# Kernel tuning notes

Hardware: AMD Instinct MI355X
Metric: run time of the kernel (lower is better)

Reference implementation:

```python
import jax, jax.numpy as jnp
import numpy as np

N = 100000
IN_CH, HID_CH, OUT_CH = 128, 128, 64
E = 1600000


def gcn_layer(x, W, b, src, dst, num_nodes):
    """PyG GCNConv: add self-loops, symmetric deg^-1/2 normalization,
    x' = D^-1/2 (A+I) D^-1/2 (x W) + b."""
    # degrees including self-loops (deg = 1 + in-degree with unit edge weights)
    ones = jnp.ones(dst.shape[0], dtype=x.dtype)
    deg = jnp.ones(num_nodes, dtype=x.dtype).at[dst].add(ones)
    dinv = jax.lax.rsqrt(deg)
    h = x @ W  # [N, out_dim] -- transform before propagate (PyG order)
    # neighbor messages
    norm = dinv[src] * dinv[dst]                      # [E]
    msg = h[src] * norm[:, None]                      # [E, out_dim] (traffic-bound)
    agg = jax.ops.segment_sum(msg, dst, num_segments=num_nodes)
    # self-loop contribution: norm_ii = dinv[i]^2
    agg = agg + h * (dinv * dinv)[:, None]
    return agg + b


def setup_inputs() -> dict:
    key = jax.random.key(0)
    ks = jax.random.split(key, 7)
    x = jax.random.normal(ks[0], (N, IN_CH), dtype=jnp.float32)
    edge_index = jax.random.randint(ks[1], (2, E), 0, N, dtype=jnp.int64)
    # Glorot-style init like PyG GCNConv
    W1 = jax.random.normal(ks[2], (IN_CH, HID_CH), dtype=jnp.float32) * (1.0 / np.sqrt(IN_CH))
    b1 = jnp.zeros((HID_CH,), dtype=jnp.float32)
    W2 = jax.random.normal(ks[3], (HID_CH, OUT_CH), dtype=jnp.float32) * (1.0 / np.sqrt(HID_CH))
    b2 = jnp.zeros((OUT_CH,), dtype=jnp.float32)
    return {"x": x, "edge_index": edge_index, "W1": W1, "b1": b1, "W2": W2, "b2": b2}


def reference(x, edge_index, W1, b1, W2, b2):
    src, dst = edge_index[0], edge_index[1]
    h = gcn_layer(x, W1, b1, src, dst, N)
    h = jax.nn.relu(h)  # dropout is identity in eval mode
    out = gcn_layer(h, W2, b2, src, dst, N)
    return out
```

## Files before the change

kernel.cpp:

```cpp
#include <hip/hip_runtime.h>
#include <hip/hip_fp16.h>

#define NNODES 100000
#define NEDGES 1600000
#define IN_C   128
#define HID_C  128
#define OUT_C  64

#define XCD_COUNT   8
#define XCD_NODES   ((NNODES + XCD_COUNT - 1) / XCD_COUNT)
#define FILL_CHUNKS 256
#define EDGES_PER_CHUNK ((NEDGES + FILL_CHUNKS - 1) / FILL_CHUNKS)

#define CAP     64
#define OVF_MAX 4096

typedef __attribute__((ext_vector_type(8))) _Float16 half8;
typedef __attribute__((ext_vector_type(4))) _Float16 half4;
typedef __attribute__((ext_vector_type(4))) float floatx4;

__device__ __forceinline__ long long load_idx(const void* p, long long i, int is64) {
  return is64 ? ((const long long*)p)[i] : (long long)((const int*)p)[i];
}

__global__ void detect_idx_kernel(const void* eidx, int* flag) {
  const unsigned* w = (const unsigned*)eidx;
  int lane = threadIdx.x & 63;
  unsigned v = w[2 * lane + 1];
  unsigned long long bad = __ballot(v != 0u);
  if (lane == 0) *flag = (bad == 0ull) ? 1 : 0;
}


__global__ void zero_cnt_kernel(int* cnt, int* ovf_cnt) {
  int i = blockIdx.x * 256 + threadIdx.x;
  if (i < NNODES) cnt[i] = 0;
  if (i == 0) *ovf_cnt = 0;
}

__global__ void compress_kernel(const void* eidx, const int* __restrict__ flag,
                                int* __restrict__ src32, int* __restrict__ dst32) {
  int e = blockIdx.x * 256 + threadIdx.x;
  if (e < NEDGES) {
    int is64 = *flag;
    src32[e] = (int)load_idx(eidx, e, is64);
    dst32[e] = (int)load_idx(eidx, (long long)NEDGES + e, is64);
  }
}

__global__ __launch_bounds__(256) void fill_fused_kernel(const int* __restrict__ src32,
                                                         const int* __restrict__ dst32,
                                                         int* __restrict__ cnt,
                                                         int* __restrict__ pad_csr,
                                                         int* __restrict__ ovf_cnt,
                                                         int2* __restrict__ ovf) {
  const int xcd = blockIdx.x & (XCD_COUNT - 1);
  const int chunk = blockIdx.x >> 3;
  const int lo = xcd * XCD_NODES;
  const int e_beg = chunk * EDGES_PER_CHUNK;
  const int e_end = min(e_beg + EDGES_PER_CHUNK, NEDGES);
  for (int e = e_beg + threadIdx.x; e < e_end; e += 256) {
    int d = __builtin_nontemporal_load(&dst32[e]);
    if ((unsigned)(d - lo) < (unsigned)XCD_NODES) {
      int s = __builtin_nontemporal_load(&src32[e]);
      int k = atomicAdd(&cnt[d], 1);
      if (k < CAP) {
        pad_csr[d * CAP + k] = s;
      } else {
        int p = atomicAdd(ovf_cnt, 1);
        if (p < OVF_MAX) ovf[p] = make_int2(s, d);
      }
    }
  }
}

__global__ void rsqrt_deg_kernel(const int* __restrict__ cnt, float* __restrict__ dinv) {
  int i = blockIdx.x * 256 + threadIdx.x;
  if (i < NNODES) dinv[i] = rsqrtf((float)(cnt[i] + 1));
}

struct F8 {
  float x0, x1, x2, x3, x4, x5, x6, x7;
};

__device__ __forceinline__ void add_h8(F8& a, const __half* p) {
  int4 r = *(const int4*)p;
  const __half2* h = (const __half2*)&r;
  float2 f0 = __half22float2(h[0]);
  float2 f1 = __half22float2(h[1]);
  float2 f2 = __half22float2(h[2]);
  float2 f3 = __half22float2(h[3]);
  a.x0 += f0.x; a.x1 += f0.y; a.x2 += f1.x; a.x3 += f1.y;
  a.x4 += f2.x; a.x5 += f2.y; a.x6 += f3.x; a.x7 += f3.y;
}

template <int C, bool RELU, bool OUT16>
__global__ __launch_bounds__(256) void gather_kernel(const int* __restrict__ cnt,
                                                     const int* __restrict__ pad_csr,
                                                     const float* __restrict__ dinv,
                                                     const __half* __restrict__ Hs,
                                                     const float* __restrict__ bias,
                                                     const int* __restrict__ ovf_cnt,
                                                     const int2* __restrict__ ovf,
                                                     void* __restrict__ OutPtr) {
  constexpr int TPN = C / 8;
  int gid = blockIdx.x * 256 + threadIdx.x;
  int i = gid / TPN;
  int c8 = (gid % TPN) * 8;
  if (i >= NNODES) return;

  const float di = dinv[i];
  const int deg = cnt[i];
  const int beg = i * CAP;
  const int end = beg + min(deg, CAP);
  const int* __restrict__ lst = pad_csr;

  F8 a0 = {}, a1 = {}, a2 = {}, a3 = {};
  add_h8(a0, &Hs[(size_t)i * C + c8]);

  int j = beg;
  for (; j + 8 <= end; j += 8) {
    int s0 = lst[j + 0], s1 = lst[j + 1], s2 = lst[j + 2], s3 = lst[j + 3];
    int s4 = lst[j + 4], s5 = lst[j + 5], s6 = lst[j + 6], s7 = lst[j + 7];
    add_h8(a0, &Hs[(size_t)s0 * C + c8]);
    add_h8(a1, &Hs[(size_t)s1 * C + c8]);
    add_h8(a2, &Hs[(size_t)s2 * C + c8]);
    add_h8(a3, &Hs[(size_t)s3 * C + c8]);
    add_h8(a0, &Hs[(size_t)s4 * C + c8]);
    add_h8(a1, &Hs[(size_t)s5 * C + c8]);
    add_h8(a2, &Hs[(size_t)s6 * C + c8]);
    add_h8(a3, &Hs[(size_t)s7 * C + c8]);
  }
  for (; j + 2 <= end; j += 2) {
    int s0 = lst[j + 0], s1 = lst[j + 1];
    add_h8(a0, &Hs[(size_t)s0 * C + c8]);
    add_h8(a1, &Hs[(size_t)s1 * C + c8]);
  }
  if (j < end) {
    add_h8(a0, &Hs[(size_t)lst[j] * C + c8]);
  }

  if (deg > CAP) {
    int n = min(*ovf_cnt, OVF_MAX);
    for (int t = 0; t < n; ++t) {
      int2 p = ovf[t];
      if (p.y == i) add_h8(a0, &Hs[(size_t)p.x * C + c8]);
    }
  }

  float s0 = a0.x0 + a1.x0 + a2.x0 + a3.x0;
  float s1 = a0.x1 + a1.x1 + a2.x1 + a3.x1;
  float s2 = a0.x2 + a1.x2 + a2.x2 + a3.x2;
  float s3 = a0.x3 + a1.x3 + a2.x3 + a3.x3;
  float s4 = a0.x4 + a1.x4 + a2.x4 + a3.x4;
  float s5 = a0.x5 + a1.x5 + a2.x5 + a3.x5;
  float s6 = a0.x6 + a1.x6 + a2.x6 + a3.x6;
  float s7 = a0.x7 + a1.x7 + a2.x7 + a3.x7;

  float4 b0 = *(const float4*)&bias[c8];
  float4 b1 = *(const float4*)&bias[c8 + 4];
  float o0 = fmaf(s0, di, b0.x);
  float o1 = fmaf(s1, di, b0.y);
  float o2 = fmaf(s2, di, b0.z);
  float o3 = fmaf(s3, di, b0.w);
  float o4 = fmaf(s4, di, b1.x);
  float o5 = fmaf(s5, di, b1.y);
  float o6 = fmaf(s6, di, b1.z);
  float o7 = fmaf(s7, di, b1.w);
  if (RELU) {
    o0 = o0 > 0.f ? o0 : 0.f;
    o1 = o1 > 0.f ? o1 : 0.f;
    o2 = o2 > 0.f ? o2 : 0.f;
    o3 = o3 > 0.f ? o3 : 0.f;
    o4 = o4 > 0.f ? o4 : 0.f;
    o5 = o5 > 0.f ? o5 : 0.f;
    o6 = o6 > 0.f ? o6 : 0.f;
    o7 = o7 > 0.f ? o7 : 0.f;
  }
  if (OUT16) {
    half8 hv = {(_Float16)o0, (_Float16)o1, (_Float16)o2, (_Float16)o3,
                (_Float16)o4, (_Float16)o5, (_Float16)o6, (_Float16)o7};
    *(half8*)((_Float16*)OutPtr + (size_t)i * C + c8) = hv;
  } else {
    float* Out = (float*)OutPtr;
    float4 v0 = make_float4(o0, o1, o2, o3);
    float4 v1 = make_float4(o4, o5, o6, o7);
    *(float4*)&Out[(size_t)i * C + c8] = v0;
    *(float4*)&Out[(size_t)i * C + c8 + 4] = v1;
  }
}

template <int K, int N, bool A_F16>
__global__ __launch_bounds__(256) void mfma_gemm_kernel(const void* __restrict__ Xv,
                                                        const float* __restrict__ Wm,
                                                        const float* __restrict__ scale,
                                                        _Float16* __restrict__ Hout,
                                                        int M) {
  constexpr int KP = K + 8;
  __shared__ alignas(16) _Float16 Alds[64 * KP];
  __shared__ alignas(16) _Float16 Wlds[N * KP];

  const int tid = threadIdx.x;
  const int row0 = blockIdx.x * 64;

  constexpr int TILES = (K / 4) * (N / 4);
  for (int tile = tid; tile < TILES; tile += 256) {
    int kt = tile / (N / 4);
    int nt = tile % (N / 4);
    const float* wp = &Wm[(4 * kt) * N + 4 * nt];
    float4 r0 = *(const float4*)(wp);
    float4 r1 = *(const float4*)(wp + N);
    float4 r2 = *(const float4*)(wp + 2 * N);
    float4 r3 = *(const float4*)(wp + 3 * N);
    half4 c0 = {(_Float16)r0.x, (_Float16)r1.x, (_Float16)r2.x, (_Float16)r3.x};
    half4 c1 = {(_Float16)r0.y, (_Float16)r1.y, (_Float16)r2.y, (_Float16)r3.y};
    half4 c2 = {(_Float16)r0.z, (_Float16)r1.z, (_Float16)r2.z, (_Float16)r3.z};
    half4 c3 = {(_Float16)r0.w, (_Float16)r1.w, (_Float16)r2.w, (_Float16)r3.w};
    *(half4*)&Wlds[(4 * nt + 0) * KP + 4 * kt] = c0;
    *(half4*)&Wlds[(4 * nt + 1) * KP + 4 * kt] = c1;
    *(half4*)&Wlds[(4 * nt + 2) * KP + 4 * kt] = c2;
    *(half4*)&Wlds[(4 * nt + 3) * KP + 4 * kt] = c3;
  }

  if (A_F16) {
    const _Float16* Xh = (const _Float16*)Xv;
    constexpr int H8PR = K / 8;
    constexpr int TOT = 64 * H8PR;
    for (int idx = tid; idx < TOT; idx += 256) {
      int lr = idx / H8PR;
      int c8 = (idx % H8PR) * 8;
      int gr = row0 + lr;
      if (gr > M - 1) gr = M - 1;
      int4 v = *(const int4*)&Xh[(size_t)gr * K + c8];
      *(int4*)&Alds[lr * KP + c8] = v;
    }
  } else {
    const float* Xf = (const float*)Xv;
    constexpr int F4PR = K / 4;
    constexpr int TOT = 64 * F4PR;
    for (int idx = tid; idx < TOT; idx += 256) {
      int lr = idx / F4PR;
      int c4 = (idx % F4PR) * 4;
      int gr = row0 + lr;
      if (gr > M - 1) gr = M - 1;
      float4 v = *(const float4*)&Xf[(size_t)gr * K + c4];
      half4 h = {(_Float16)v.x, (_Float16)v.y, (_Float16)v.z, (_Float16)v.w};
      *(half4*)&Alds[lr * KP + c4] = h;
    }
  }
  __syncthreads();

  const int w = tid >> 6;
  const int lane = tid & 63;
  const int g = lane >> 4;
  const int mi = lane & 15;
  constexpr int NT = N / 16;

  floatx4 acc[NT];
#pragma unroll
  for (int t = 0; t < NT; ++t) acc[t] = (floatx4){0.f, 0.f, 0.f, 0.f};

  const _Float16* arow = &Alds[(w * 16 + mi) * KP];
#pragma unroll
  for (int ks = 0; ks < K / 32; ++ks) {
    half8 a = *(const half8*)(arow + ks * 32 + g * 8);
#pragma unroll
    for (int t = 0; t < NT; ++t) {
      half8 b = *(const half8*)&Wlds[(t * 16 + mi) * KP + ks * 32 + g * 8];
      acc[t] = __builtin_amdgcn_mfma_f32_16x16x32_f16(a, b, acc[t], 0, 0, 0);
    }
  }

#pragma unroll
  for (int r = 0; r < 4; ++r) {
    int grow = row0 + w * 16 + 4 * g + r;
    if (grow < M) {
      float s = scale[grow];
      _Float16* orow = Hout + (size_t)grow * N + mi;
#pragma unroll
      for (int t = 0; t < NT; ++t) orow[t * 16] = (_Float16)(acc[t][r] * s);
    }
  }
}

extern "C" void kernel_launch(void* const* d_in, const int* in_sizes, int n_in,
                              void* d_out, int out_size, void* d_ws, size_t ws_size,
                              hipStream_t stream) {
  const float* x = (const float*)d_in[0];
  const void* eidx = d_in[1];
  const float* W1 = (const float*)d_in[2];
  const float* b1 = (const float*)d_in[3];
  const float* W2 = (const float*)d_in[4];
  const float* b2 = (const float*)d_in[5];
  float* out = (float*)d_out;
  char* ws = (char*)d_ws;

  int*   flag    = (int*)(ws + 0);
  int*   ovf_cnt = (int*)(ws + 512);
  int*   cnt     = (int*)(ws + 1024);
  float* dinv    = (float*)(ws + 401408);
  int2*  ovf     = (int2*)(ws + 801792);
  int*   src32   = (int*)(ws + 835072);
  int*   dst32   = (int*)(ws + 7235584);
  int*   pad_csr = (int*)(ws + 13636096);
  _Float16* h1   = (_Float16*)(ws + 39236608);
  _Float16* hidden = (_Float16*)(ws + 64837120);
  _Float16* h2 = h1;

  detect_idx_kernel<<<1, 64, 0, stream>>>(eidx, flag);
  zero_cnt_kernel<<<(NNODES + 255) / 256, 256, 0, stream>>>(cnt, ovf_cnt);
  compress_kernel<<<(NEDGES + 255) / 256, 256, 0, stream>>>(eidx, flag, src32, dst32);
  fill_fused_kernel<<<XCD_COUNT * FILL_CHUNKS, 256, 0, stream>>>(src32, dst32, cnt,
                                                                 pad_csr, ovf_cnt, ovf);
  rsqrt_deg_kernel<<<(NNODES + 255) / 256, 256, 0, stream>>>(cnt, dinv);

  const int GB = (NNODES + 63) / 64;

  mfma_gemm_kernel<IN_C, HID_C, false>
      <<<GB, 256, 0, stream>>>(x, W1, dinv, h1, NNODES);
  gather_kernel<HID_C, true, true>
      <<<(NNODES * (HID_C / 8) + 255) / 256, 256, 0, stream>>>(cnt, pad_csr, dinv,
                                                               (const __half*)h1, b1,
                                                               ovf_cnt, ovf, hidden);
  mfma_gemm_kernel<HID_C, OUT_C, true>
      <<<GB, 256, 0, stream>>>(hidden, W2, dinv, h2, NNODES);
  gather_kernel<OUT_C, false, false>
      <<<(NNODES * (OUT_C / 8) + 255) / 256, 256, 0, stream>>>(cnt, pad_csr, dinv,
                                                               (const __half*)h2, b2,
                                                               ovf_cnt, ovf, out);
}
```

Baseline: 318.5 us.

## Build padded CSR via two-pass bucket binning with shared-memory assembly

Replaces the compress kernel and the XCD-partitioned scatter fill with a two-pass build. The first pass bins edges into 128-node buckets using packed src/local-dst words. The second pass assembles each bucket's padded adjacency in LDS and writes it out with coalesced int4 stores. The goal is to cut global atomic contention and random scattered writes to pad_csr, and to drop the separate src32/dst32 pass. In exchange it adds a staging buffer, a bucket-overflow path with a fixup kernel, and a 17-bit source packing limit.

```diff
diff --git a/kernel.cpp b/kernel.cpp
--- a/kernel.cpp
+++ b/kernel.cpp
@@ -7,13 +7,13 @@
 #define HID_C  128
 #define OUT_C  64
 
-#define XCD_COUNT   8
-#define XCD_NODES   ((NNODES + XCD_COUNT - 1) / XCD_COUNT)
-#define FILL_CHUNKS 256
-#define EDGES_PER_CHUNK ((NEDGES + FILL_CHUNKS - 1) / FILL_CHUNKS)
-
 #define CAP     64
 #define OVF_MAX 4096
+
+#define BUCKET_SHIFT 7
+#define BUCKET_NODES 128
+#define NB ((NNODES + BUCKET_NODES - 1) / BUCKET_NODES)
+#define BCAP 3072
 
 typedef __attribute__((ext_vector_type(8))) _Float16 half8;
 typedef __attribute__((ext_vector_type(4))) _Float16 half4;
@@ -32,44 +32,88 @@
 }
 
 
-__global__ void zero_cnt_kernel(int* cnt, int* ovf_cnt) {
+__global__ void zero_misc_kernel(int* bcnt, int* ovf_cnt, int* ovfA_cnt) {
   int i = blockIdx.x * 256 + threadIdx.x;
-  if (i < NNODES) cnt[i] = 0;
-  if (i == 0) *ovf_cnt = 0;
-}
-
-__global__ void compress_kernel(const void* eidx, const int* __restrict__ flag,
-                                int* __restrict__ src32, int* __restrict__ dst32) {
+  if (i < NB) bcnt[i] = 0;
+  if (i == 0) { *ovf_cnt = 0; *ovfA_cnt = 0; }
+}
+
+__global__ __launch_bounds__(256) void binA_kernel(const void* __restrict__ eidx,
+                                                   const int* __restrict__ flag,
+                                                   int* __restrict__ bcnt,
+                                                   unsigned* __restrict__ buf,
+                                                   int* __restrict__ ovfA_cnt,
+                                                   int2* __restrict__ ovfA) {
   int e = blockIdx.x * 256 + threadIdx.x;
-  if (e < NEDGES) {
-    int is64 = *flag;
-    src32[e] = (int)load_idx(eidx, e, is64);
-    dst32[e] = (int)load_idx(eidx, (long long)NEDGES + e, is64);
-  }
-}
-
-__global__ __launch_bounds__(256) void fill_fused_kernel(const int* __restrict__ src32,
-                                                         const int* __restrict__ dst32,
-                                                         int* __restrict__ cnt,
-                                                         int* __restrict__ pad_csr,
-                                                         int* __restrict__ ovf_cnt,
-                                                         int2* __restrict__ ovf) {
-  const int xcd = blockIdx.x & (XCD_COUNT - 1);
-  const int chunk = blockIdx.x >> 3;
-  const int lo = xcd * XCD_NODES;
-  const int e_beg = chunk * EDGES_PER_CHUNK;
-  const int e_end = min(e_beg + EDGES_PER_CHUNK, NEDGES);
-  for (int e = e_beg + threadIdx.x; e < e_end; e += 256) {
-    int d = __builtin_nontemporal_load(&dst32[e]);
-    if ((unsigned)(d - lo) < (unsigned)XCD_NODES) {
-      int s = __builtin_nontemporal_load(&src32[e]);
-      int k = atomicAdd(&cnt[d], 1);
-      if (k < CAP) {
-        pad_csr[d * CAP + k] = s;
-      } else {
-        int p = atomicAdd(ovf_cnt, 1);
-        if (p < OVF_MAX) ovf[p] = make_int2(s, d);
-      }
+  if (e >= NEDGES) return;
+  int is64 = *flag;
+  int s = (int)load_idx(eidx, e, is64);
+  int d = (int)load_idx(eidx, (long long)NEDGES + e, is64);
+  int b = d >> BUCKET_SHIFT;
+  int k = atomicAdd(&bcnt[b], 1);
+  if (k < BCAP) {
+    buf[(size_t)b * BCAP + k] = (unsigned)s | ((unsigned)(d & (BUCKET_NODES - 1)) << 17);
+  } else {
+    int p = atomicAdd(ovfA_cnt, 1);
+    if (p < OVF_MAX) ovfA[p] = make_int2(s, d);
+  }
+}
+
+__global__ __launch_bounds__(256) void binB_kernel(const int* __restrict__ bcnt,
+                                                   const unsigned* __restrict__ buf,
+                                                   int* __restrict__ cnt,
+                                                   int* __restrict__ pad_csr,
+                                                   int* __restrict__ ovf_cnt,
+                                                   int2* __restrict__ ovf) {
+  __shared__ int pad[BUCKET_NODES * CAP];
+  __shared__ int lcnt[BUCKET_NODES];
+  const int b = blockIdx.x;
+  const int tid = threadIdx.x;
+  const int node0 = b << BUCKET_SHIFT;
+
+  if (tid < BUCKET_NODES) lcnt[tid] = 0;
+  __syncthreads();
+
+  const int n = min(bcnt[b], BCAP);
+  for (int k = tid; k < n; k += 256) {
+    unsigned u = buf[(size_t)b * BCAP + k];
+    int s = (int)(u & 0x1FFFFu);
+    int dl = (int)(u >> 17);
+    int slot = atomicAdd(&lcnt[dl], 1);
+    if (slot < CAP) {
+      pad[dl * CAP + slot] = s;
+    } else {
+      int p = atomicAdd(ovf_cnt, 1);
+      if (p < OVF_MAX) ovf[p] = make_int2(s, node0 + dl);
+    }
+  }
+  __syncthreads();
+
+  constexpr int I4PN = CAP / 4;
+  for (int q = tid; q < BUCKET_NODES * I4PN; q += 256) {
+    int dl = q / I4PN;
+    int gn = node0 + dl;
+    if (gn < NNODES) {
+      int c = (q % I4PN) * 4;
+      *(int4*)&pad_csr[(size_t)gn * CAP + c] = *(const int4*)&pad[dl * CAP + c];
+    }
+  }
+  if (tid < BUCKET_NODES && node0 + tid < NNODES) cnt[node0 + tid] = lcnt[tid];
+}
+
+__global__ void fixup_kernel(const int* __restrict__ ovfA_cnt,
+                             const int2* __restrict__ ovfA,
+                             int* __restrict__ cnt, int* __restrict__ pad_csr,
+                             int* __restrict__ ovf_cnt, int2* __restrict__ ovf) {
+  int n = min(*ovfA_cnt, OVF_MAX);
+  for (int t = blockIdx.x * 256 + threadIdx.x; t < n; t += gridDim.x * 256) {
+    int2 p = ovfA[t];
+    int k = atomicAdd(&cnt[p.y], 1);
+    if (k < CAP) {
+      pad_csr[(size_t)p.y * CAP + k] = p.x;
+    } else {
+      int q = atomicAdd(ovf_cnt, 1);
+      if (q < OVF_MAX) ovf[q] = p;
     }
   }
 }
@@ -295,23 +339,26 @@
   float* out = (float*)d_out;
   char* ws = (char*)d_ws;
 
-  int*   flag    = (int*)(ws + 0);
-  int*   ovf_cnt = (int*)(ws + 512);
-  int*   cnt     = (int*)(ws + 1024);
-  float* dinv    = (float*)(ws + 401408);
-  int2*  ovf     = (int2*)(ws + 801792);
-  int*   src32   = (int*)(ws + 835072);
-  int*   dst32   = (int*)(ws + 7235584);
-  int*   pad_csr = (int*)(ws + 13636096);
-  _Float16* h1   = (_Float16*)(ws + 39236608);
-  _Float16* hidden = (_Float16*)(ws + 64837120);
+  int*      flag     = (int*)(ws + 0);
+  int*      ovf_cnt  = (int*)(ws + 512);
+  int*      ovfA_cnt = (int*)(ws + 1024);
+  int*      bcnt     = (int*)(ws + 1536);
+  int*      cnt      = (int*)(ws + 8192);
+  float*    dinv     = (float*)(ws + 408576);
+  int2*     ovf      = (int2*)(ws + 809472);
+  int2*     ovfA     = (int2*)(ws + 842752);
+  unsigned* buf      = (unsigned*)(ws + 876032);
+  int*      pad_csr  = (int*)(ws + 10510336);
+  _Float16* h1       = (_Float16*)(ws + 36110848);
+  _Float16* hidden   = (_Float16*)(ws + 61711360);
   _Float16* h2 = h1;
 
   detect_idx_kernel<<<1, 64, 0, stream>>>(eidx, flag);
-  zero_cnt_kernel<<<(NNODES + 255) / 256, 256, 0, stream>>>(cnt, ovf_cnt);
-  compress_kernel<<<(NEDGES + 255) / 256, 256, 0, stream>>>(eidx, flag, src32, dst32);
-  fill_fused_kernel<<<XCD_COUNT * FILL_CHUNKS, 256, 0, stream>>>(src32, dst32, cnt,
-                                                                 pad_csr, ovf_cnt, ovf);
+  zero_misc_kernel<<<(NB + 255) / 256, 256, 0, stream>>>(bcnt, ovf_cnt, ovfA_cnt);
+  binA_kernel<<<(NEDGES + 255) / 256, 256, 0, stream>>>(eidx, flag, bcnt, buf,
+                                                        ovfA_cnt, ovfA);
+  binB_kernel<<<NB, 256, 0, stream>>>(bcnt, buf, cnt, pad_csr, ovf_cnt, ovf);
+  fixup_kernel<<<1, 256, 0, stream>>>(ovfA_cnt, ovfA, cnt, pad_csr, ovf_cnt, ovf);
   rsqrt_deg_kernel<<<(NNODES + 255) / 256, 256, 0, stream>>>(cnt, dinv);
 
   const int GB = (NNODES + 63) / 64;
```

After: 625.9 us. 96.5% more time.
